# Kernel tuning notes

Hardware: AMD Instinct MI355X
Metric: run time of the kernel (lower is better)

## Reference

```python
import jax, jax.numpy as jnp
import numpy as np

NUM_POS = 4
N = 8192
C = 4096  # number of identity classes == logit dim


def setup_inputs() -> dict:
    key = jax.random.key(0)
    k1, k2 = jax.random.split(key)
    feat = jax.random.normal(k1, (N, C), dtype=jnp.float32)
    label = jax.random.randint(k2, (N,), 0, C, dtype=jnp.int64)
    return {"feat": feat, "label": label}


def reference(feat, label):
    # feat: [n, C] logits, label: [n] int class ids.
    n, c = feat.shape
    # Segment-mean replaces the O(n^2) masked-mean loop:
    # center[i] = mean of feat over all j with label[j] == label[i]
    sums = jax.ops.segment_sum(feat, label, num_segments=c)              # [C, C]
    counts = jax.ops.segment_sum(jnp.ones((n,), feat.dtype), label,
                                 num_segments=c)                          # [C]
    center = sums[label] / counts[label][:, None]                         # [n, C]
    # CrossEntropyLoss (mean reduction) on centers as logits
    logp = jax.nn.log_softmax(center, axis=-1)
    ce = -jnp.take_along_axis(logp, label[:, None], axis=1)[:, 0].mean()
    m = n / NUM_POS
    return ce / m
```

## Files before the change

kernel.cpp:

```cpp
#include <hip/hip_runtime.h>
#include <math.h>

#define NN 8192
#define CC 4096
#define SLOTS 64
#define BLK 256

#define SCALE (4.0f / (8192.0f * 8192.0f))

__global__ void init_kernel(int* __restrict__ counts) {
    int i = blockIdx.x * blockDim.x + threadIdx.x;
    if (i < CC) counts[i] = 0;
}

__global__ void build_index(const int* __restrict__ label,
                            int* __restrict__ counts,
                            int* __restrict__ lists) {
    int i = blockIdx.x * blockDim.x + threadIdx.x;
    if (i < NN) {
        int lab = label[i];
        int pos = atomicAdd(&counts[lab], 1);
        if (pos < SLOTS) lists[lab * SLOTS + pos] = i;
    }
}

__global__ __launch_bounds__(BLK) void class_loss(const float* __restrict__ feat,
                                                  const int* __restrict__ counts,
                                                  const int* __restrict__ lists,
                                                  float* __restrict__ value) {
    int c = blockIdx.x;
    int t = threadIdx.x;
    int lane = t & 63, w = t >> 6;

    __shared__ int s_cnt;
    __shared__ int s_rows[SLOTS];
    if (t == 0) s_cnt = counts[c];
    if (t < SLOTS) s_rows[t] = lists[c * SLOTS + t];
    __syncthreads();

    int cnt = s_cnt;
    if (cnt == 0) {
        if (t == 0) value[c] = 0.0f;
        return;
    }
    int m = cnt < SLOTS ? cnt : SLOTS;

    float4 a[4];
    #pragma unroll
    for (int i = 0; i < 4; ++i) a[i] = make_float4(0.f, 0.f, 0.f, 0.f);

    int base_slot = w * 256 + lane;
    int r0 = s_rows[0];

    for (int k = 0; k < m; k += 4) {
        int ra = s_rows[k];
        int rb = (k + 1 < m) ? s_rows[k + 1] : r0;
        int rc = (k + 2 < m) ? s_rows[k + 2] : r0;
        int rd = (k + 3 < m) ? s_rows[k + 3] : r0;
        float fb = (k + 1 < m) ? 1.f : 0.f;
        float fc = (k + 2 < m) ? 1.f : 0.f;
        float fd = (k + 3 < m) ? 1.f : 0.f;
        const float4* pa = (const float4*)(feat + (size_t)ra * CC);
        const float4* pb = (const float4*)(feat + (size_t)rb * CC);
        const float4* pc = (const float4*)(feat + (size_t)rc * CC);
        const float4* pd = (const float4*)(feat + (size_t)rd * CC);

        float4 va[4], vb[4], vc4[4], vd[4];
        #pragma unroll
        for (int i = 0; i < 4; ++i) va[i] = pa[base_slot + i * 64];
        #pragma unroll
        for (int i = 0; i < 4; ++i) vb[i] = pb[base_slot + i * 64];
        #pragma unroll
        for (int i = 0; i < 4; ++i) vc4[i] = pc[base_slot + i * 64];
        #pragma unroll
        for (int i = 0; i < 4; ++i) vd[i] = pd[base_slot + i * 64];

        #pragma unroll
        for (int i = 0; i < 4; ++i) {
            a[i].x += va[i].x + fb * vb[i].x + fc * vc4[i].x + fd * vd[i].x;
            a[i].y += va[i].y + fb * vb[i].y + fc * vc4[i].y + fd * vd[i].y;
            a[i].z += va[i].z + fb * vb[i].z + fc * vc4[i].z + fd * vd[i].z;
            a[i].w += va[i].w + fb * vb[i].w + fc * vc4[i].w + fd * vd[i].w;
        }
    }

    float inv = 1.0f / (float)cnt;
    float vals[16];
    #pragma unroll
    for (int i = 0; i < 4; ++i) {
        vals[i * 4 + 0] = a[i].x * inv;
        vals[i * 4 + 1] = a[i].y * inv;
        vals[i * 4 + 2] = a[i].z * inv;
        vals[i * 4 + 3] = a[i].w * inv;
    }

    __shared__ float s_red[4];
    __shared__ float s_bcast;
    __shared__ float s_vc;

    float wm = vals[0];
    #pragma unroll
    for (int j = 1; j < 16; ++j) wm = fmaxf(wm, vals[j]);
    #pragma unroll
    for (int off = 1; off < 64; off <<= 1) wm = fmaxf(wm, __shfl_xor(wm, off, 64));
    if (lane == 0) s_red[w] = wm;
    __syncthreads();
    if (t == 0) s_bcast = fmaxf(fmaxf(s_red[0], s_red[1]), fmaxf(s_red[2], s_red[3]));
    __syncthreads();
    float M = s_bcast;

    int s_idx = c >> 2, cj = c & 3;
    int ow = s_idx >> 8, orem = s_idx & 255;
    int oi = orem >> 6, ol = orem & 63;
    float se = 0.f;
    #pragma unroll
    for (int j = 0; j < 16; ++j) se += __expf(vals[j] - M);
    #pragma unroll
    for (int off = 1; off < 64; off <<= 1) se += __shfl_xor(se, off, 64);
    if (lane == 0) s_red[w] = se;
    if (t == ow * 64 + ol) s_vc = vals[oi * 4 + cj];
    __syncthreads();

    if (t == 0) {
        float S = s_red[0] + s_red[1] + s_red[2] + s_red[3];
        value[c] = (float)cnt * (M + __logf(S) - s_vc);
    }
}

__global__ __launch_bounds__(BLK) void finalize(const float* __restrict__ value,
                                                float* __restrict__ out) {
    int t = threadIdx.x;
    const float4* v4 = (const float4*)value;
    float s = 0.f;
    #pragma unroll
    for (int i = 0; i < CC / 4 / BLK; ++i) {
        float4 v = v4[i * BLK + t];
        s += v.x + v.y + v.z + v.w;
    }
    #pragma unroll
    for (int off = 1; off < 64; off <<= 1) s += __shfl_xor(s, off, 64);
    __shared__ float s_red[4];
    int lane = t & 63, wv = t >> 6;
    if (lane == 0) s_red[wv] = s;
    __syncthreads();
    if (t == 0) out[0] = (s_red[0] + s_red[1] + s_red[2] + s_red[3]) * SCALE;
}

extern "C" void kernel_launch(void* const* d_in, const int* in_sizes, int n_in,
                              void* d_out, int out_size, void* d_ws, size_t ws_size,
                              hipStream_t stream) {
    const float* feat = (const float*)d_in[0];
    const int* label = (const int*)d_in[1];
    float* out = (float*)d_out;

    int* counts = (int*)d_ws;
    int* lists = counts + CC;
    float* value = (float*)(lists + CC * SLOTS);

    init_kernel<<<(CC + BLK - 1) / BLK, BLK, 0, stream>>>(counts);
    build_index<<<(NN + BLK - 1) / BLK, BLK, 0, stream>>>(label, counts, lists);
    class_loss<<<CC, BLK, 0, stream>>>(feat, counts, lists, value);
    finalize<<<1, BLK, 0, stream>>>(value, out);
}
```

Baseline: 203.9 us.

## Replace per-class gather with atomic scatter-add into dense class sum matrix

Swaps the per-class index lists and row gathers for a dense CxC sum matrix. Rows of feat are scattered into it with float atomics, then a per-class log-sum-exp pass reads it. This removes the SLOTS cap on rows per class and the irregular gather loop. In exchange it adds a 64 MB zeroing pass, 33M float atomics and a 64 MB re-read, so memory traffic roughly triples, and the result becomes nondeterministic.

```diff
diff --git a/kernel.cpp b/kernel.cpp
--- a/kernel.cpp
+++ b/kernel.cpp
@@ -3,95 +3,75 @@
 
 #define NN 8192
 #define CC 4096
-#define SLOTS 64
 #define BLK 256
 
 #define SCALE (4.0f / (8192.0f * 8192.0f))
 
-__global__ void init_kernel(int* __restrict__ counts) {
-    int i = blockIdx.x * blockDim.x + threadIdx.x;
-    if (i < CC) counts[i] = 0;
+__global__ __launch_bounds__(BLK) void zero_kernel(float4* __restrict__ sums4,
+                                                   int4* __restrict__ counts4) {
+    int gid = blockIdx.x * BLK + threadIdx.x;
+    float4 z = make_float4(0.f, 0.f, 0.f, 0.f);
+    #pragma unroll
+    for (int i = 0; i < 8; ++i)
+        sums4[(size_t)i * 524288 + gid] = z;
+    if (gid < CC / 4) counts4[gid] = make_int4(0, 0, 0, 0);
 }
 
-__global__ void build_index(const int* __restrict__ label,
-                            int* __restrict__ counts,
-                            int* __restrict__ lists) {
+__global__ void build_counts(const int* __restrict__ label, int* __restrict__ counts) {
     int i = blockIdx.x * blockDim.x + threadIdx.x;
-    if (i < NN) {
-        int lab = label[i];
-        int pos = atomicAdd(&counts[lab], 1);
-        if (pos < SLOTS) lists[lab * SLOTS + pos] = i;
+    if (i < NN) atomicAdd(&counts[label[i]], 1);
+}
+
+__global__ __launch_bounds__(BLK) void scatter_kernel(const float4* __restrict__ f4,
+                                                      const int* __restrict__ label,
+                                                      float* __restrict__ sums) {
+    int idx = blockIdx.x * BLK + threadIdx.x;
+    int col4 = idx & 1023;
+    int row0 = idx >> 10;
+
+    float4 v[16];
+    #pragma unroll
+    for (int i = 0; i < 16; ++i)
+        v[i] = f4[(size_t)i * 524288 + idx];
+
+    #pragma unroll
+    for (int i = 0; i < 16; ++i) {
+        int lab = label[row0 + i * 512];
+        float* dst = sums + (size_t)lab * CC + col4 * 4;
+        unsafeAtomicAdd(dst + 0, v[i].x);
+        unsafeAtomicAdd(dst + 1, v[i].y);
+        unsafeAtomicAdd(dst + 2, v[i].z);
+        unsafeAtomicAdd(dst + 3, v[i].w);
     }
 }
 
-__global__ __launch_bounds__(BLK) void class_loss(const float* __restrict__ feat,
+__global__ __launch_bounds__(BLK) void lse_kernel(const float* __restrict__ sums,
                                                   const int* __restrict__ counts,
-                                                  const int* __restrict__ lists,
-                                                  float* __restrict__ value) {
+                                                  float* __restrict__ wval) {
     int c = blockIdx.x;
     int t = threadIdx.x;
     int lane = t & 63, w = t >> 6;
 
-    __shared__ int s_cnt;
-    __shared__ int s_rows[SLOTS];
-    if (t == 0) s_cnt = counts[c];
-    if (t < SLOTS) s_rows[t] = lists[c * SLOTS + t];
-    __syncthreads();
-
-    int cnt = s_cnt;
+    int cnt = counts[c];
     if (cnt == 0) {
-        if (t == 0) value[c] = 0.0f;
+        if (t == 0) wval[c] = 0.0f;
         return;
     }
-    int m = cnt < SLOTS ? cnt : SLOTS;
 
-    float4 a[4];
+    const float4* row4 = (const float4*)(sums + (size_t)c * CC);
+    int base_slot = w * 256 + lane;
+    float4 v[4];
     #pragma unroll
-    for (int i = 0; i < 4; ++i) a[i] = make_float4(0.f, 0.f, 0.f, 0.f);
-
-    int base_slot = w * 256 + lane;
-    int r0 = s_rows[0];
-
-    for (int k = 0; k < m; k += 4) {
-        int ra = s_rows[k];
-        int rb = (k + 1 < m) ? s_rows[k + 1] : r0;
-        int rc = (k + 2 < m) ? s_rows[k + 2] : r0;
-        int rd = (k + 3 < m) ? s_rows[k + 3] : r0;
-        float fb = (k + 1 < m) ? 1.f : 0.f;
-        float fc = (k + 2 < m) ? 1.f : 0.f;
-        float fd = (k + 3 < m) ? 1.f : 0.f;
-        const float4* pa = (const float4*)(feat + (size_t)ra * CC);
-        const float4* pb = (const float4*)(feat + (size_t)rb * CC);
-        const float4* pc = (const float4*)(feat + (size_t)rc * CC);
-        const float4* pd = (const float4*)(feat + (size_t)rd * CC);
-
-        float4 va[4], vb[4], vc4[4], vd[4];
-        #pragma unroll
-        for (int i = 0; i < 4; ++i) va[i] = pa[base_slot + i * 64];
-        #pragma unroll
-        for (int i = 0; i < 4; ++i) vb[i] = pb[base_slot + i * 64];
-        #pragma unroll
-        for (int i = 0; i < 4; ++i) vc4[i] = pc[base_slot + i * 64];
-        #pragma unroll
-        for (int i = 0; i < 4; ++i) vd[i] = pd[base_slot + i * 64];
-
-        #pragma unroll
-        for (int i = 0; i < 4; ++i) {
-            a[i].x += va[i].x + fb * vb[i].x + fc * vc4[i].x + fd * vd[i].x;
-            a[i].y += va[i].y + fb * vb[i].y + fc * vc4[i].y + fd * vd[i].y;
-            a[i].z += va[i].z + fb * vb[i].z + fc * vc4[i].z + fd * vd[i].z;
-            a[i].w += va[i].w + fb * vb[i].w + fc * vc4[i].w + fd * vd[i].w;
-        }
-    }
+    for (int i = 0; i < 4; ++i) v[i] = row4[base_slot + i * 64];
 
     float inv = 1.0f / (float)cnt;
     float vals[16];
     #pragma unroll
     for (int i = 0; i < 4; ++i) {
-        vals[i * 4 + 0] = a[i].x * inv;
-        vals[i * 4 + 1] = a[i].y * inv;
-        vals[i * 4 + 2] = a[i].z * inv;
-        vals[i * 4 + 3] = a[i].w * inv;
+        vals[i * 4 + 0] = v[i].x * inv;
+        vals[i * 4 + 1] = v[i].y * inv;
+        vals[i * 4 + 2] = v[i].z * inv;
+        vals[i * 4 + 3] = v[i].w * inv;
     }
 
     __shared__ float s_red[4];
@@ -123,14 +103,14 @@
 
     if (t == 0) {
         float S = s_red[0] + s_red[1] + s_red[2] + s_red[3];
-        value[c] = (float)cnt * (M + __logf(S) - s_vc);
+        wval[c] = (float)cnt * (M + __logf(S) - s_vc);
     }
 }
 
-__global__ __launch_bounds__(BLK) void finalize(const float* __restrict__ value,
-                                                float* __restrict__ out) {
+__global__ __launch_bounds__(BLK) void final_kernel(const float* __restrict__ wval,
+                                                    float* __restrict__ out) {
     int t = threadIdx.x;
-    const float4* v4 = (const float4*)value;
+    const float4* v4 = (const float4*)wval;
     float s = 0.f;
     #pragma unroll
     for (int i = 0; i < CC / 4 / BLK; ++i) {
@@ -140,8 +120,8 @@
     #pragma unroll
     for (int off = 1; off < 64; off <<= 1) s += __shfl_xor(s, off, 64);
     __shared__ float s_red[4];
-    int lane = t & 63, wv = t >> 6;
-    if (lane == 0) s_red[wv] = s;
+    int lane = t & 63, w = t >> 6;
+    if (lane == 0) s_red[w] = s;
     __syncthreads();
     if (t == 0) out[0] = (s_red[0] + s_red[1] + s_red[2] + s_red[3]) * SCALE;
 }
@@ -153,12 +133,13 @@
     const int* label = (const int*)d_in[1];
     float* out = (float*)d_out;
 
-    int* counts = (int*)d_ws;
-    int* lists = counts + CC;
-    float* value = (float*)(lists + CC * SLOTS);
+    float* sums = (float*)d_ws;
+    int* counts = (int*)(sums + (size_t)CC * CC);
+    float* wval = (float*)(counts + CC);
 
-    init_kernel<<<(CC + BLK - 1) / BLK, BLK, 0, stream>>>(counts);
-    build_index<<<(NN + BLK - 1) / BLK, BLK, 0, stream>>>(label, counts, lists);
-    class_loss<<<CC, BLK, 0, stream>>>(feat, counts, lists, value);
-    finalize<<<1, BLK, 0, stream>>>(value, out);
+    zero_kernel<<<2048, BLK, 0, stream>>>((float4*)sums, (int4*)counts);
+    build_counts<<<NN / BLK, BLK, 0, stream>>>(label, counts);
+    scatter_kernel<<<2048, BLK, 0, stream>>>((const float4*)feat, label, sums);
+    lse_kernel<<<CC, BLK, 0, stream>>>(sums, counts, wval);
+    final_kernel<<<1, BLK, 0, stream>>>(wval, out);
 }
```

New measurement: 601.7 us. +195.2%, slower.
